# Kernel tuning notes

Hardware: AMD Instinct MI355X
Metric: run time of the kernel (lower is better)

## Reference

```python
import jax, jax.numpy as jnp
import numpy as np

N_NODES = 50000
N_EDGES = 1600000
HIDDEN = 128
SPATIAL = 3
SCORE_HIDDEN = 128
EPS = 1e-12


def setup_inputs() -> dict:
    key = jax.random.key(0)
    ks = jax.random.split(key, 12)
    s = 0.02
    return {
        "h": jax.random.normal(ks[0], (N_NODES, HIDDEN), dtype=jnp.float32),
        "edge_index": jax.random.randint(ks[1], (2, N_EDGES), 0, N_NODES, dtype=jnp.int64),
        "rel_pos": jax.random.normal(ks[2], (N_EDGES, SPATIAL), dtype=jnp.float32),
        "distance": jax.random.uniform(ks[3], (N_EDGES, 1), dtype=jnp.float32),
        "node_weight": jax.random.uniform(ks[4], (N_NODES,), dtype=jnp.float32),
        "W1": jax.random.normal(ks[5], (2 * HIDDEN + SPATIAL + 1, SCORE_HIDDEN), dtype=jnp.float32) * s,
        "b1": jnp.zeros((SCORE_HIDDEN,), dtype=jnp.float32),
        "W2": jax.random.normal(ks[6], (SCORE_HIDDEN, SCORE_HIDDEN), dtype=jnp.float32) * s,
        "b2": jnp.zeros((SCORE_HIDDEN,), dtype=jnp.float32),
        "W3": jax.random.normal(ks[7], (SCORE_HIDDEN, 1), dtype=jnp.float32) * s,
        "b3": jnp.zeros((1,), dtype=jnp.float32),
        "Wv": jax.random.normal(ks[8], (HIDDEN, HIDDEN), dtype=jnp.float32) * s,
    }


def reference(h, edge_index, rel_pos, distance, node_weight, W1, b1, W2, b2, W3, b3, Wv):
    num_nodes = h.shape[0]
    dst, src = edge_index[0], edge_index[1]
    # per-edge gathered feature: [E, 2*H + spatial + 1]
    edge_feat = jnp.concatenate([h[dst], h[src], rel_pos, distance], axis=-1)
    # 3-layer score MLP -> scalar score per edge
    x = jax.nn.silu(edge_feat @ W1 + b1)
    x = jax.nn.silu(x @ W2 + b2)
    scores = (x @ W3 + b3)[:, 0]  # [E]
    # edge softmax over incoming edges of each dst node
    mx = jax.ops.segment_max(scores, dst, num_segments=num_nodes)  # -inf for empty segments
    exp_scores = jnp.exp(scores - mx[dst])
    den = jax.ops.segment_sum(exp_scores, dst, num_segments=num_nodes)
    alpha = exp_scores / (den[dst] + EPS)
    # value projection, weighted message, scatter-add aggregation
    msg = (h[src] @ Wv) * (alpha * node_weight[src])[:, None]
    out = jax.ops.segment_sum(msg, dst, num_segments=num_nodes)
    return h + out
```

## Files before the change

kernel.cpp:

```cpp
#include <hip/hip_runtime.h>
#include <hip/hip_bf16.h>
#include <cstdint>
#include <cstddef>

#define N_NODES 50000
#define N_EDGES 1600000
#define HID 128
#define PCAT_N 384
#define EPSV 1e-12f

typedef __bf16 bf16_t;
typedef __bf16 bf16x8 __attribute__((ext_vector_type(8)));
typedef float f32x4 __attribute__((ext_vector_type(4)));

__device__ __forceinline__ float bf2f_lo(unsigned u) {
    return __builtin_bit_cast(float, u << 16);
}
__device__ __forceinline__ float bf2f_hi(unsigned u) {
    return __builtin_bit_cast(float, u & 0xFFFF0000u);
}
__device__ __forceinline__ unsigned short f2bf_rne(float x) {
    unsigned u = __builtin_bit_cast(unsigned, x);
    u += 0x7FFFu + ((u >> 16) & 1u);
    return (unsigned short)(u >> 16);
}
__device__ __forceinline__ float silu_f(float x) {
    return x * __builtin_amdgcn_rcpf(1.0f + __expf(-x));
}

__global__ void k_prepw(const float* __restrict__ W1, const float* __restrict__ W2,
                        const float* __restrict__ Wv, bf16_t* __restrict__ wcatT,
                        bf16_t* __restrict__ w2t) {
    int idx = blockIdx.x * blockDim.x + threadIdx.x;
    if (idx < 384 * 128) {
        int n = idx >> 7, k = idx & 127;
        float v;
        if (n < 128)      v = W1[k * 128 + n];
        else if (n < 256) v = W1[(128 + k) * 128 + (n - 128)];
        else              v = Wv[k * 128 + (n - 256)];
        wcatT[idx] = __builtin_bit_cast(bf16_t, f2bf_rne(v));
    } else if (idx < 384 * 128 + 128 * 128) {
        int j = idx - 384 * 128;
        int n = j >> 7, k = j & 127;
        w2t[j] = __builtin_bit_cast(bf16_t, f2bf_rne(W2[k * 128 + n]));
    }
}

__global__ __launch_bounds__(256) void k_nodeproj(
    const float* __restrict__ h, const bf16_t* __restrict__ wcatT,
    const float* __restrict__ nw, bf16_t* __restrict__ pcat) {
    __shared__ bf16_t As[64 * 136];
    int t = threadIdx.x;
    int r0 = blockIdx.x * 64;
    {
        int r = t >> 2, cbase = (t & 3) * 32;
        int gr = r0 + r;
        if (gr >= N_NODES) gr = 0;
        const float* src = h + (size_t)gr * 128 + cbase;
        bf16_t* dst = As + r * 136 + cbase;
#pragma unroll
        for (int i = 0; i < 4; ++i) {
            float4 v0 = *reinterpret_cast<const float4*>(src + i * 8);
            float4 v1 = *reinterpret_cast<const float4*>(src + i * 8 + 4);
            uint4 pk;
            pk.x = (unsigned)f2bf_rne(v0.x) | ((unsigned)f2bf_rne(v0.y) << 16);
            pk.y = (unsigned)f2bf_rne(v0.z) | ((unsigned)f2bf_rne(v0.w) << 16);
            pk.z = (unsigned)f2bf_rne(v1.x) | ((unsigned)f2bf_rne(v1.y) << 16);
            pk.w = (unsigned)f2bf_rne(v1.z) | ((unsigned)f2bf_rne(v1.w) << 16);
            *reinterpret_cast<uint4*>(dst + i * 8) = pk;
        }
    }
    __syncthreads();
    int lane = t & 63, w = t >> 6;
    f32x4 acc[4][6] = {};
#pragma unroll
    for (int kk = 0; kk < 4; ++kk) {
        bf16x8 af[4], bfr[6];
#pragma unroll
        for (int fm = 0; fm < 4; ++fm)
            af[fm] = *reinterpret_cast<const bf16x8*>(
                As + (fm * 16 + (lane & 15)) * 136 + kk * 32 + (lane >> 4) * 8);
#pragma unroll
        for (int fn = 0; fn < 6; ++fn) {
            int n = w * 96 + fn * 16 + (lane & 15);
            bfr[fn] = *reinterpret_cast<const bf16x8*>(
                wcatT + (size_t)n * 128 + kk * 32 + (lane >> 4) * 8);
        }
#pragma unroll
        for (int fm = 0; fm < 4; ++fm)
#pragma unroll
            for (int fn = 0; fn < 6; ++fn)
                acc[fm][fn] = __builtin_amdgcn_mfma_f32_16x16x32_bf16(
                    af[fm], bfr[fn], acc[fm][fn], 0, 0, 0);
    }
#pragma unroll
    for (int fm = 0; fm < 4; ++fm) {
#pragma unroll
        for (int j = 0; j < 4; ++j) {
            int row = r0 + fm * 16 + (lane >> 4) * 4 + j;
            if (row < N_NODES) {
                float nwv = (w >= 2) ? nw[row] : 1.0f;
#pragma unroll
                for (int fn = 0; fn < 6; ++fn) {
                    int colbase = w * 96 + fn * 16;
                    float v = acc[fm][fn][j];
                    if (colbase >= 256) v *= nwv;
                    pcat[(size_t)row * PCAT_N + colbase + (lane & 15)] =
                        __builtin_bit_cast(bf16_t, f2bf_rne(v));
                }
            }
        }
    }
}

__global__ void k_hist(const int* __restrict__ eidx, int* __restrict__ hist) {
    int stride = gridDim.x * blockDim.x;
    for (int e = blockIdx.x * blockDim.x + threadIdx.x; e < N_EDGES; e += stride)
        atomicAdd(&hist[eidx[e]], 1);
}

__global__ __launch_bounds__(1024) void k_scan(const int* __restrict__ hist,
                                               int* __restrict__ row_start,
                                               int* __restrict__ cursor,
                                               float* __restrict__ den) {
    __shared__ int partial[1024];
    int t = threadIdx.x;
    const int C = (N_NODES + 1023) / 1024;
    int base = t * C;
    int sum = 0;
    for (int i = 0; i < C; ++i) {
        int j = base + i;
        if (j < N_NODES) sum += hist[j];
    }
    partial[t] = sum;
    __syncthreads();
    for (int off = 1; off < 1024; off <<= 1) {
        int v = (t >= off) ? partial[t - off] : 0;
        __syncthreads();
        partial[t] += v;
        __syncthreads();
    }
    int run = partial[t] - sum;
    for (int i = 0; i < C; ++i) {
        int j = base + i;
        if (j < N_NODES) {
            row_start[j] = run;
            cursor[j] = run;
            den[j] = 0.0f;
            run += hist[j];
        }
    }
    if (t == 1023) row_start[N_NODES] = partial[1023];
}

__global__ void k_scatter(const int* __restrict__ eidx, int* __restrict__ cursor,
                          int* __restrict__ perm) {
    int stride = gridDim.x * blockDim.x;
    for (int e = blockIdx.x * blockDim.x + threadIdx.x; e < N_EDGES; e += stride) {
        int d = eidx[e];
        int pos = atomicAdd(&cursor[d], 1);
        perm[pos] = e;
    }
}

__global__ __launch_bounds__(256, 6) void k_edge(
    const bf16_t* __restrict__ pcat, const bf16_t* __restrict__ w2t,
    const int* __restrict__ perm, const int* __restrict__ eidx,
    const float* __restrict__ rel_pos, const float* __restrict__ dist,
    const float* __restrict__ W1, const float* __restrict__ b1,
    const float* __restrict__ b2, const float* __restrict__ W3,
    const float* __restrict__ b3, float* __restrict__ escore,
    int* __restrict__ src_csr, float* __restrict__ den) {
    __shared__ bf16_t Ax[64 * 136];
    __shared__ int s_dst[64];
    __shared__ int s_src[64];
    __shared__ float4 s_rp[64];
    __shared__ float s_sc[64];

    int t = threadIdx.x;
    int e0 = blockIdx.x * 64;
    if (t < 64) {
        int e = perm[e0 + t];
        s_dst[t] = eidx[e];
        s_src[t] = eidx[N_EDGES + e];
        s_rp[t] = make_float4(rel_pos[(size_t)e * 3], rel_pos[(size_t)e * 3 + 1],
                              rel_pos[(size_t)e * 3 + 2], dist[e]);
        s_sc[t] = b3[0];
    }
    int lane = t & 63, w = t >> 6;
    int c0 = 2 * lane;
    float wA0 = W1[256 * 128 + c0], wA1 = W1[257 * 128 + c0];
    float wA2 = W1[258 * 128 + c0], wA3 = W1[259 * 128 + c0];
    float bA = b1[c0];
    float wB0 = W1[256 * 128 + c0 + 1], wB1 = W1[257 * 128 + c0 + 1];
    float wB2 = W1[258 * 128 + c0 + 1], wB3 = W1[259 * 128 + c0 + 1];
    float bB = b1[c0 + 1];
    __syncthreads();

#pragma unroll 4
    for (int i = 0; i < 16; ++i) {
        int e = w * 16 + i;
        int dn = s_dst[e], sn = s_src[e];
        float4 rp = s_rp[e];
        unsigned pa = *reinterpret_cast<const unsigned*>(pcat + (size_t)dn * PCAT_N + c0);
        unsigned pb = *reinterpret_cast<const unsigned*>(pcat + (size_t)sn * PCAT_N + 128 + c0);
        float x0 = bf2f_lo(pa) + bf2f_lo(pb) +
                   rp.x * wA0 + rp.y * wA1 + rp.z * wA2 + rp.w * wA3 + bA;
        float x1 = bf2f_hi(pa) + bf2f_hi(pb) +
                   rp.x * wB0 + rp.y * wB1 + rp.z * wB2 + rp.w * wB3 + bB;
        float y0 = silu_f(x0), y1 = silu_f(x1);
        unsigned pk = (unsigned)f2bf_rne(y0) | ((unsigned)f2bf_rne(y1) << 16);
        *reinterpret_cast<unsigned*>(Ax + e * 136 + c0) = pk;
    }
    __syncthreads();

    f32x4 acc[4][2] = {};
#pragma unroll
    for (int kk = 0; kk < 4; ++kk) {
        bf16x8 af[4], bfr[2];
#pragma unroll
        for (int fn = 0; fn < 2; ++fn) {
            int n = w * 32 + fn * 16 + (lane & 15);
            bfr[fn] = *reinterpret_cast<const bf16x8*>(
                w2t + (size_t)n * 128 + kk * 32 + (lane >> 4) * 8);
        }
#pragma unroll
        for (int fm = 0; fm < 4; ++fm)
            af[fm] = *reinterpret_cast<const bf16x8*>(
                Ax + (fm * 16 + (lane & 15)) * 136 + kk * 32 + (lane >> 4) * 8);
#pragma unroll
        for (int fm = 0; fm < 4; ++fm)
#pragma unroll
            for (int fn = 0; fn < 2; ++fn)
                acc[fm][fn] = __builtin_amdgcn_mfma_f32_16x16x32_bf16(
                    af[fm], bfr[fn], acc[fm][fn], 0, 0, 0);
    }

    float w3v[2], b2v[2];
#pragma unroll
    for (int fn = 0; fn < 2; ++fn) {
        int n = w * 32 + fn * 16 + (lane & 15);
        w3v[fn] = W3[n];
        b2v[fn] = b2[n];
    }
#pragma unroll
    for (int fm = 0; fm < 4; ++fm) {
        float pj[4] = {0.f, 0.f, 0.f, 0.f};
#pragma unroll
        for (int fn = 0; fn < 2; ++fn) {
#pragma unroll
            for (int j = 0; j < 4; ++j)
                pj[j] += silu_f(acc[fm][fn][j] + b2v[fn]) * w3v[fn];
        }
#pragma unroll
        for (int j = 0; j < 4; ++j) {
            float v = pj[j];
            v += __shfl_xor(v, 1);
            v += __shfl_xor(v, 2);
            v += __shfl_xor(v, 4);
            v += __shfl_xor(v, 8);
            if ((lane & 15) == 0)
                atomicAdd(&s_sc[fm * 16 + (lane >> 4) * 4 + j], v);
        }
    }
    __syncthreads();

    if (t < 64) {
        float esc = __expf(s_sc[t]);
        escore[e0 + t] = esc;
        src_csr[e0 + t] = s_src[t];
        int d = s_dst[t];
        float v = esc;
#pragma unroll
        for (int off = 1; off <= 32; off <<= 1) {
            float ov = __shfl_up(v, (unsigned)off);
            int od = __shfl_up(d, (unsigned)off);
            if (t >= off && od == d) v += ov;
        }
        bool end = (t == 63) || (s_dst[t + 1] != d);
        if (end) atomicAdd(&den[d], v);
    }
}

__global__ __launch_bounds__(256) void k_agg(
    const float* __restrict__ h, const bf16_t* __restrict__ pcat,
    const float* __restrict__ escore, const int* __restrict__ src_csr,
    const int* __restrict__ row_start, const float* __restrict__ den,
    float* __restrict__ out) {
    __shared__ float s_coef[4][64];
    __shared__ int s_sv[4][64];
    int t = threadIdx.x, lane = t & 63, w = t >> 6;
    int node = blockIdx.x * 4 + w;
    if (node >= N_NODES) return;
    int s = row_start[node];
    int deg = row_start[node + 1] - s;
    float acc0 = 0.f, acc1 = 0.f;
    if (deg > 0) {
        float inv = __builtin_amdgcn_rcpf(den[node] + EPSV);
        for (int base = 0; base < deg; base += 64) {
            int i = base + lane;
            if (i < deg) {
                s_coef[w][lane] = escore[s + i] * inv;
                s_sv[w][lane] = src_csr[s + i];
            }
            asm volatile("s_waitcnt lgkmcnt(0)" ::: "memory");
            int m = deg - base;
            if (m > 64) m = 64;
#pragma unroll 4
            for (int j = 0; j < m; ++j) {
                float c = s_coef[w][j];
                int sv = s_sv[w][j];
                unsigned hv = *reinterpret_cast<const unsigned*>(
                    pcat + (size_t)sv * PCAT_N + 256 + 2 * lane);
                acc0 += c * bf2f_lo(hv);
                acc1 += c * bf2f_hi(hv);
            }
            asm volatile("s_waitcnt lgkmcnt(0)" ::: "memory");
        }
    }
    size_t o = (size_t)node * 128 + 2 * lane;
    float2 hv2 = *reinterpret_cast<const float2*>(h + o);
    float2 res;
    res.x = hv2.x + acc0;
    res.y = hv2.y + acc1;
    *reinterpret_cast<float2*>(out + o) = res;
}

extern "C" void kernel_launch(void* const* d_in, const int* in_sizes, int n_in,
                              void* d_out, int out_size, void* d_ws, size_t ws_size,
                              hipStream_t stream) {
    const float* h       = (const float*)d_in[0];
    const int*   eidx    = (const int*)d_in[1];
    const float* rel_pos = (const float*)d_in[2];
    const float* dist    = (const float*)d_in[3];
    const float* nw      = (const float*)d_in[4];
    const float* W1      = (const float*)d_in[5];
    const float* b1      = (const float*)d_in[6];
    const float* W2      = (const float*)d_in[7];
    const float* b2      = (const float*)d_in[8];
    const float* W3      = (const float*)d_in[9];
    const float* b3      = (const float*)d_in[10];
    const float* Wv      = (const float*)d_in[11];
    float* out = (float*)d_out;

    char* p = (char*)d_ws;
    auto carve = [&](size_t bytes) {
        char* r = p;
        p += (bytes + 255) & ~(size_t)255;
        return r;
    };
    bf16_t* pcat    = (bf16_t*)carve((size_t)N_NODES * PCAT_N * 2);
    bf16_t* wcatT   = (bf16_t*)carve(384 * 128 * 2);
    bf16_t* w2t     = (bf16_t*)carve(128 * 128 * 2);
    float* escore   = (float*)carve((size_t)N_EDGES * 4);
    int* src_csr    = (int*)carve((size_t)N_EDGES * 4);
    int* perm       = (int*)carve((size_t)N_EDGES * 4);
    int* hist       = (int*)carve((size_t)N_NODES * 4);
    int* row_start  = (int*)carve((size_t)(N_NODES + 1) * 4);
    int* cursor     = (int*)carve((size_t)N_NODES * 4);
    float* den      = (float*)carve((size_t)N_NODES * 4);

    hipMemsetAsync(hist, 0, (size_t)N_NODES * 4, stream);
    k_prepw<<<256, 256, 0, stream>>>(W1, W2, Wv, wcatT, w2t);
    k_nodeproj<<<(N_NODES + 63) / 64, 256, 0, stream>>>(h, wcatT, nw, pcat);
    k_hist<<<2048, 256, 0, stream>>>(eidx, hist);
    k_scan<<<1, 1024, 0, stream>>>(hist, row_start, cursor, den);
    k_scatter<<<2048, 256, 0, stream>>>(eidx, cursor, perm);
    k_edge<<<N_EDGES / 64, 256, 0, stream>>>(pcat, w2t, perm, eidx, rel_pos,
                                             dist, W1, b1, b2, W3, b3,
                                             escore, src_csr, den);
    k_agg<<<(N_NODES + 3) / 4, 256, 0, stream>>>(h, pcat, escore, src_csr,
                                                 row_start, den, out);
}
```

Baseline: 770.4 us.

## Fuse edge scoring with aggregation and pack per-edge records during scatter

```diff
diff --git a/kernel.cpp b/kernel.cpp
--- a/kernel.cpp
+++ b/kernel.cpp
@@ -153,38 +153,52 @@
     if (t == 1023) row_start[N_NODES] = partial[1023];
 }
 
-__global__ void k_scatter(const int* __restrict__ eidx, int* __restrict__ cursor,
-                          int* __restrict__ perm) {
+__global__ void k_scatter(const int* __restrict__ eidx,
+                          const float* __restrict__ rel_pos,
+                          const float* __restrict__ dist,
+                          int* __restrict__ cursor,
+                          uint4* __restrict__ recs) {
     int stride = gridDim.x * blockDim.x;
     for (int e = blockIdx.x * blockDim.x + threadIdx.x; e < N_EDGES; e += stride) {
         int d = eidx[e];
+        int sv = eidx[N_EDGES + e];
+        float r0 = rel_pos[(size_t)e * 3];
+        float r1 = rel_pos[(size_t)e * 3 + 1];
+        float r2 = rel_pos[(size_t)e * 3 + 2];
+        float dd = dist[e];
+        uint4 rec;
+        rec.x = (unsigned)f2bf_rne(r0) | ((unsigned)f2bf_rne(r1) << 16);
+        rec.y = (unsigned)f2bf_rne(r2) | ((unsigned)f2bf_rne(dd) << 16);
+        rec.z = (unsigned)d;
+        rec.w = (unsigned)sv;
         int pos = atomicAdd(&cursor[d], 1);
-        perm[pos] = e;
-    }
-}
-
-__global__ __launch_bounds__(256, 6) void k_edge(
+        recs[pos] = rec;
+    }
+}
+
+__global__ __launch_bounds__(256, 6) void k_fused(
     const bf16_t* __restrict__ pcat, const bf16_t* __restrict__ w2t,
-    const int* __restrict__ perm, const int* __restrict__ eidx,
-    const float* __restrict__ rel_pos, const float* __restrict__ dist,
-    const float* __restrict__ W1, const float* __restrict__ b1,
-    const float* __restrict__ b2, const float* __restrict__ W3,
-    const float* __restrict__ b3, float* __restrict__ escore,
-    int* __restrict__ src_csr, float* __restrict__ den) {
+    const uint4* __restrict__ recs, const float* __restrict__ W1,
+    const float* __restrict__ b1, const float* __restrict__ b2,
+    const float* __restrict__ W3, const float* __restrict__ b3,
+    float* __restrict__ den, float* __restrict__ outp) {
     __shared__ bf16_t Ax[64 * 136];
     __shared__ int s_dst[64];
     __shared__ int s_src[64];
     __shared__ float4 s_rp[64];
     __shared__ float s_sc[64];
+    __shared__ int s_runstart[65];
+    __shared__ int s_runnode[64];
+    __shared__ int s_nruns;
 
     int t = threadIdx.x;
     int e0 = blockIdx.x * 64;
     if (t < 64) {
-        int e = perm[e0 + t];
-        s_dst[t] = eidx[e];
-        s_src[t] = eidx[N_EDGES + e];
-        s_rp[t] = make_float4(rel_pos[(size_t)e * 3], rel_pos[(size_t)e * 3 + 1],
-                              rel_pos[(size_t)e * 3 + 2], dist[e]);
+        uint4 rec = recs[e0 + t];
+        s_dst[t] = (int)rec.z;
+        s_src[t] = (int)rec.w;
+        s_rp[t] = make_float4(bf2f_lo(rec.x), bf2f_hi(rec.x),
+                              bf2f_lo(rec.y), bf2f_hi(rec.y));
         s_sc[t] = b3[0];
     }
     int lane = t & 63, w = t >> 6;
@@ -196,6 +210,21 @@
     float wB2 = W1[258 * 128 + c0 + 1], wB3 = W1[259 * 128 + c0 + 1];
     float bB = b1[c0 + 1];
     __syncthreads();
+
+    if (t < 64) {
+        bool flag = (t == 0) || (s_dst[t] != s_dst[t - 1]);
+        unsigned long long mask = __ballot((int)flag);
+        int rid = (int)__popcll(mask & ((2ull << t) - 1)) - 1;
+        if (flag) {
+            s_runstart[rid] = t;
+            s_runnode[rid] = s_dst[t];
+        }
+        if (t == 0) {
+            int nr = (int)__popcll(mask);
+            s_nruns = nr;
+            s_runstart[nr] = 64;
+        }
+    }
 
 #pragma unroll 4
     for (int i = 0; i < 16; ++i) {
@@ -265,65 +294,38 @@
     }
     __syncthreads();
 
-    if (t < 64) {
-        float esc = __expf(s_sc[t]);
-        escore[e0 + t] = esc;
-        src_csr[e0 + t] = s_src[t];
-        int d = s_dst[t];
-        float v = esc;
-#pragma unroll
-        for (int off = 1; off <= 32; off <<= 1) {
-            float ov = __shfl_up(v, (unsigned)off);
-            int od = __shfl_up(d, (unsigned)off);
-            if (t >= off && od == d) v += ov;
-        }
-        bool end = (t == 63) || (s_dst[t + 1] != d);
-        if (end) atomicAdd(&den[d], v);
-    }
-}
-
-__global__ __launch_bounds__(256) void k_agg(
-    const float* __restrict__ h, const bf16_t* __restrict__ pcat,
-    const float* __restrict__ escore, const int* __restrict__ src_csr,
-    const int* __restrict__ row_start, const float* __restrict__ den,
-    float* __restrict__ out) {
-    __shared__ float s_coef[4][64];
-    __shared__ int s_sv[4][64];
-    int t = threadIdx.x, lane = t & 63, w = t >> 6;
-    int node = blockIdx.x * 4 + w;
-    if (node >= N_NODES) return;
-    int s = row_start[node];
-    int deg = row_start[node + 1] - s;
-    float acc0 = 0.f, acc1 = 0.f;
-    if (deg > 0) {
-        float inv = __builtin_amdgcn_rcpf(den[node] + EPSV);
-        for (int base = 0; base < deg; base += 64) {
-            int i = base + lane;
-            if (i < deg) {
-                s_coef[w][lane] = escore[s + i] * inv;
-                s_sv[w][lane] = src_csr[s + i];
-            }
-            asm volatile("s_waitcnt lgkmcnt(0)" ::: "memory");
-            int m = deg - base;
-            if (m > 64) m = 64;
-#pragma unroll 4
-            for (int j = 0; j < m; ++j) {
-                float c = s_coef[w][j];
-                int sv = s_sv[w][j];
-                unsigned hv = *reinterpret_cast<const unsigned*>(
-                    pcat + (size_t)sv * PCAT_N + 256 + 2 * lane);
-                acc0 += c * bf2f_lo(hv);
-                acc1 += c * bf2f_hi(hv);
-            }
-            asm volatile("s_waitcnt lgkmcnt(0)" ::: "memory");
-        }
-    }
-    size_t o = (size_t)node * 128 + 2 * lane;
-    float2 hv2 = *reinterpret_cast<const float2*>(h + o);
+    int nruns = s_nruns;
+    for (int r = w; r < nruns; r += 4) {
+        int node = s_runnode[r];
+        int j0 = s_runstart[r], j1 = s_runstart[r + 1];
+        float a0 = 0.f, a1 = 0.f, ad = 0.f;
+        for (int j = j0; j < j1; ++j) {
+            float c = __expf(s_sc[j]);
+            int sv = s_src[j];
+            unsigned hv = *reinterpret_cast<const unsigned*>(
+                pcat + (size_t)sv * PCAT_N + 256 + c0);
+            a0 += c * bf2f_lo(hv);
+            a1 += c * bf2f_hi(hv);
+            ad += c;
+        }
+        atomicAdd(&outp[(size_t)node * 128 + c0], a0);
+        atomicAdd(&outp[(size_t)node * 128 + c0 + 1], a1);
+        if (lane == 0) atomicAdd(&den[node], ad);
+    }
+}
+
+__global__ __launch_bounds__(256) void k_norm(const float* __restrict__ h,
+                                              const float* __restrict__ den,
+                                              float* __restrict__ outp) {
+    int idx = blockIdx.x * 256 + threadIdx.x;
+    int node = idx >> 6;
+    float inv = __builtin_amdgcn_rcpf(den[node] + EPSV);
+    float2 n2 = *reinterpret_cast<const float2*>(outp + (size_t)idx * 2);
+    float2 h2 = *reinterpret_cast<const float2*>(h + (size_t)idx * 2);
     float2 res;
-    res.x = hv2.x + acc0;
-    res.y = hv2.y + acc1;
-    *reinterpret_cast<float2*>(out + o) = res;
+    res.x = h2.x + n2.x * inv;
+    res.y = h2.y + n2.y * inv;
+    *reinterpret_cast<float2*>(outp + (size_t)idx * 2) = res;
 }
 
 extern "C" void kernel_launch(void* const* d_in, const int* in_sizes, int n_in,
@@ -352,23 +354,20 @@
     bf16_t* pcat    = (bf16_t*)carve((size_t)N_NODES * PCAT_N * 2);
     bf16_t* wcatT   = (bf16_t*)carve(384 * 128 * 2);
     bf16_t* w2t     = (bf16_t*)carve(128 * 128 * 2);
-    float* escore   = (float*)carve((size_t)N_EDGES * 4);
-    int* src_csr    = (int*)carve((size_t)N_EDGES * 4);
-    int* perm       = (int*)carve((size_t)N_EDGES * 4);
+    uint4* recs     = (uint4*)carve((size_t)N_EDGES * 16);
     int* hist       = (int*)carve((size_t)N_NODES * 4);
     int* row_start  = (int*)carve((size_t)(N_NODES + 1) * 4);
     int* cursor     = (int*)carve((size_t)N_NODES * 4);
     float* den      = (float*)carve((size_t)N_NODES * 4);
 
     hipMemsetAsync(hist, 0, (size_t)N_NODES * 4, stream);
+    hipMemsetAsync(out, 0, (size_t)N_NODES * HID * 4, stream);
     k_prepw<<<256, 256, 0, stream>>>(W1, W2, Wv, wcatT, w2t);
     k_nodeproj<<<(N_NODES + 63) / 64, 256, 0, stream>>>(h, wcatT, nw, pcat);
     k_hist<<<2048, 256, 0, stream>>>(eidx, hist);
     k_scan<<<1, 1024, 0, stream>>>(hist, row_start, cursor, den);
-    k_scatter<<<2048, 256, 0, stream>>>(eidx, cursor, perm);
-    k_edge<<<N_EDGES / 64, 256, 0, stream>>>(pcat, w2t, perm, eidx, rel_pos,
-                                             dist, W1, b1, b2, W3, b3,
-                                             escore, src_csr, den);
-    k_agg<<<(N_NODES + 3) / 4, 256, 0, stream>>>(h, pcat, escore, src_csr,
-                                                 row_start, den, out);
-}
+    k_scatter<<<2048, 256, 0, stream>>>(eidx, rel_pos, dist, cursor, recs);
+    k_fused<<<N_EDGES / 64, 256, 0, stream>>>(pcat, w2t, recs, W1, b1, b2,
+                                              W3, b3, den, out);
+    k_norm<<<(N_NODES * HID / 2) / 256, 256, 0, stream>>>(h, den, out);
+}
```

New measurement: 783.2 us. Within noise of the previous version (+1.7%).
